# Optimization experiments

Measured on AMD Instinct MI355X. Metric: run time of the kernel, lower is better.

The kernel has to match this reference:

```python
import jax, jax.numpy as jnp
import numpy as np

LOG2 = 0.6931471805599453  # shifted_softplus(x) = softplus(x) - log(2)
NUM_MOL = 20_000  # static maxm for segment reduction


def ssp(x):
    return jax.nn.softplus(x) - LOG2


def setup_inputs() -> dict:
    key = jax.random.key(0)
    ks = jax.random.split(key, 5)
    N, D, H, E, M = 1_000_000, 128, 64, 4, NUM_MOL
    x = jax.random.normal(ks[0], (N, D), dtype=jnp.float32)
    zidx = jax.random.randint(ks[1], (N,), 0, E, dtype=jnp.int32)
    idx_m = jnp.sort(jax.random.randint(ks[2], (N,), 0, M, dtype=jnp.int32))
    # stacked per-element pyramidal MLP params: D -> D//2 -> 1
    W1 = jax.random.normal(ks[3], (E, D, H), dtype=jnp.float32) * (1.0 / np.sqrt(D))
    b1 = jnp.zeros((E, H), dtype=jnp.float32)
    W2 = jax.random.normal(ks[4], (E, H, 1), dtype=jnp.float32) * (1.0 / np.sqrt(H))
    b2 = jnp.zeros((E, 1), dtype=jnp.float32)
    return dict(x=x, zidx=zidx, idx_m=idx_m, W1=W1, b1=b1, W2=W2, b2=b2)


def reference(x, zidx, idx_m, W1, b1, W2, b2):
    # ElementwiseMLP: run each element's 2-layer MLP, select per atom by element.
    E = W1.shape[0]
    yi = jnp.zeros((x.shape[0], W2.shape[-1]), dtype=x.dtype)  # [N, n_out]
    for e in range(E):  # small fixed element set
        h = ssp(x @ W1[e] + b1[e])            # [N, H]
        ye = h @ W2[e] + b2[e]                # [N, n_out]
        yi = yi + jnp.where((zidx == e)[:, None], ye, jnp.zeros((), dtype=x.dtype))
    # aggregation_mode == 'sum': index_add per molecule
    y = jax.ops.segment_sum(yi, idx_m, num_segments=NUM_MOL)  # [M, n_out]
    return jnp.squeeze(y, -1)  # [M]
```

## Files before the change

kernel.cpp:

```cpp
#include <hip/hip_runtime.h>

typedef _Float16 half8 __attribute__((ext_vector_type(8)));
typedef float f32x4 __attribute__((ext_vector_type(4)));

#define LDSROW 136

__global__ __launch_bounds__(256, 2)
void elemental_atomwise_kernel(const float* __restrict__ x,
                               const int* __restrict__ zidx,
                               const int* __restrict__ idx_m,
                               const float* __restrict__ W1,
                               const float* __restrict__ b1,
                               const float* __restrict__ W2,
                               const float* __restrict__ b2,
                               float* __restrict__ y,
                               int N) {
  extern __shared__ _Float16 w1t[];

#pragma unroll
  for (int it = 0; it < 32; ++it) {
    int idx4 = threadIdx.x + it * 256;
    f32x4 v = ((const f32x4*)W1)[idx4];
    int lin = idx4 << 2;
    int e = lin >> 13;
    int d = (lin >> 6) & 127;
    int h = lin & 63;
    int n = e * 64 + h;
#pragma unroll
    for (int j = 0; j < 4; ++j)
      w1t[(n + j) * LDSROW + d] = (_Float16)v[j];
  }
  __syncthreads();

  const int lane = threadIdx.x & 63;
  const int wave = threadIdx.x >> 6;
  const int c = lane & 15;
  const int q = lane >> 4;
  const long tile = (long)blockIdx.x * 4 + wave;
  const long base = tile * 64;
  if (base >= N) return;

  int ameta = (base + lane < N) ? (int)(base + lane) : (N - 1);
  const int zvec = zidx[ameta];
  const int ivec = idx_m[ameta];

  half8 af[4][4];
#pragma unroll
  for (int mt = 0; mt < 4; ++mt) {
    long row = base + mt * 16 + c;
    if (row >= N) row = N - 1;
    const f32x4* rp = (const f32x4*)(x + row * 128);
#pragma unroll
    for (int kt = 0; kt < 4; ++kt) {
      f32x4 u0 = rp[kt * 8 + q * 2];
      f32x4 u1 = rp[kt * 8 + q * 2 + 1];
      half8 a;
      a[0] = (_Float16)u0[0]; a[1] = (_Float16)u0[1];
      a[2] = (_Float16)u0[2]; a[3] = (_Float16)u0[3];
      a[4] = (_Float16)u1[0]; a[5] = (_Float16)u1[1];
      a[6] = (_Float16)u1[2]; a[7] = (_Float16)u1[3];
      af[mt][kt] = a;
    }
  }

#pragma unroll
  for (int e = 0; e < 4; ++e) {
    f32x4 acc[4][4];
#pragma unroll
    for (int mt = 0; mt < 4; ++mt)
#pragma unroll
      for (int nt = 0; nt < 4; ++nt)
        acc[mt][nt] = (f32x4){0.f, 0.f, 0.f, 0.f};

#pragma unroll
    for (int kt = 0; kt < 4; ++kt) {
#pragma unroll
      for (int nt = 0; nt < 4; ++nt) {
        half8 bf = *(const half8*)&w1t[(e * 64 + nt * 16 + c) * LDSROW + kt * 32 + q * 8];
#pragma unroll
        for (int mt = 0; mt < 4; ++mt)
          acc[mt][nt] = __builtin_amdgcn_mfma_f32_16x16x32_f16(af[mt][kt], bf, acc[mt][nt], 0, 0, 0);
      }
    }

    float b1v[4], w2v[4];
#pragma unroll
    for (int nt = 0; nt < 4; ++nt) {
      b1v[nt] = b1[e * 64 + nt * 16 + c];
      w2v[nt] = W2[e * 64 + nt * 16 + c];
    }
    const float b2e = b2[e];
#pragma unroll
    for (int mt = 0; mt < 4; ++mt) {
#pragma unroll
      for (int i = 0; i < 4; ++i) {
        float s = 0.0f;
#pragma unroll
        for (int nt = 0; nt < 4; ++nt) {
          float t = acc[mt][nt][i] + b1v[nt];
          float hsp = __logf(1.0f + __expf(t)) - 0.69314718056f;
          s = fmaf(hsp, w2v[nt], s);
        }
        s += __shfl_xor(s, 1);
        s += __shfl_xor(s, 2);
        s += __shfl_xor(s, 4);
        s += __shfl_xor(s, 8);
        int mloc = mt * 16 + q * 4 + i;
        int zm = __shfl(zvec, mloc);
        int im = __shfl(ivec, mloc);
        if (c == 0 && zm == e && base + mloc < N)
          atomicAdd(&y[im], s + b2e);
      }
    }
  }
}

extern "C" void kernel_launch(void* const* d_in, const int* in_sizes, int n_in,
                              void* d_out, int out_size, void* d_ws, size_t ws_size,
                              hipStream_t stream) {
  const float* x = (const float*)d_in[0];
  const int* zidx = (const int*)d_in[1];
  const int* idx_m = (const int*)d_in[2];
  const float* W1 = (const float*)d_in[3];
  const float* b1 = (const float*)d_in[4];
  const float* W2 = (const float*)d_in[5];
  const float* b2 = (const float*)d_in[6];
  float* y = (float*)d_out;

  const int N = in_sizes[0] / 128;

  hipMemsetAsync(d_out, 0, (size_t)out_size * sizeof(float), stream);

  const int tiles = (N + 63) / 64;
  const int blocks = (tiles + 3) / 4;
  const size_t lds_bytes = 256 * LDSROW * sizeof(_Float16);

  elemental_atomwise_kernel<<<blocks, 256, lds_bytes, stream>>>(
      x, zidx, idx_m, W1, b1, W2, b2, y, N);
}
```

Measured before the change: 836.0 us.

## Assign one element per wave with register-resident weights and persistent grid

Changes the work split so each of the four waves in a block owns one element's W1 slice, held in registers as fp16 fragments, and all four waves process the same 64-atom tile. A persistent grid of 512 blocks strides over tiles, so the LDS staging of W1 and the per-block prologue are paid once per block rather than once per 64×4 atoms. The costs are that each x tile is now read by four waves (relying on L2/L1 reuse), every wave computes only its element, register pressure rises from 64 extra VGPRs of weight fragments, and the strided per-element W1 global loads are uncoalesced at startup.

```diff
diff --git a/kernel.cpp b/kernel.cpp
--- a/kernel.cpp
+++ b/kernel.cpp
@@ -2,8 +2,6 @@
 
 typedef _Float16 half8 __attribute__((ext_vector_type(8)));
 typedef float f32x4 __attribute__((ext_vector_type(4)));
-
-#define LDSROW 136
 
 __global__ __launch_bounds__(256, 2)
 void elemental_atomwise_kernel(const float* __restrict__ x,
@@ -14,57 +12,39 @@
                                const float* __restrict__ W2,
                                const float* __restrict__ b2,
                                float* __restrict__ y,
-                               int N) {
-  extern __shared__ _Float16 w1t[];
-
-#pragma unroll
-  for (int it = 0; it < 32; ++it) {
-    int idx4 = threadIdx.x + it * 256;
-    f32x4 v = ((const f32x4*)W1)[idx4];
-    int lin = idx4 << 2;
-    int e = lin >> 13;
-    int d = (lin >> 6) & 127;
-    int h = lin & 63;
-    int n = e * 64 + h;
-#pragma unroll
-    for (int j = 0; j < 4; ++j)
-      w1t[(n + j) * LDSROW + d] = (_Float16)v[j];
-  }
-  __syncthreads();
-
+                               int N, int ntiles) {
   const int lane = threadIdx.x & 63;
-  const int wave = threadIdx.x >> 6;
+  const int e = threadIdx.x >> 6;
   const int c = lane & 15;
   const int q = lane >> 4;
-  const long tile = (long)blockIdx.x * 4 + wave;
-  const long base = tile * 64;
-  if (base >= N) return;
 
-  int ameta = (base + lane < N) ? (int)(base + lane) : (N - 1);
-  const int zvec = zidx[ameta];
-  const int ivec = idx_m[ameta];
+  half8 bf[4][4];
+#pragma unroll
+  for (int kt = 0; kt < 4; ++kt)
+#pragma unroll
+    for (int nt = 0; nt < 4; ++nt) {
+      const float* wp = W1 + e * 8192 + (kt * 32 + q * 8) * 64 + nt * 16 + c;
+      half8 b;
+#pragma unroll
+      for (int j = 0; j < 8; ++j) b[j] = (_Float16)wp[j * 64];
+      bf[kt][nt] = b;
+    }
+  float b1v[4], w2v[4];
+#pragma unroll
+  for (int nt = 0; nt < 4; ++nt) {
+    b1v[nt] = b1[e * 64 + nt * 16 + c];
+    w2v[nt] = W2[e * 64 + nt * 16 + c];
+  }
+  const float b2e = b2[e];
 
-  half8 af[4][4];
-#pragma unroll
-  for (int mt = 0; mt < 4; ++mt) {
-    long row = base + mt * 16 + c;
-    if (row >= N) row = N - 1;
-    const f32x4* rp = (const f32x4*)(x + row * 128);
-#pragma unroll
-    for (int kt = 0; kt < 4; ++kt) {
-      f32x4 u0 = rp[kt * 8 + q * 2];
-      f32x4 u1 = rp[kt * 8 + q * 2 + 1];
-      half8 a;
-      a[0] = (_Float16)u0[0]; a[1] = (_Float16)u0[1];
-      a[2] = (_Float16)u0[2]; a[3] = (_Float16)u0[3];
-      a[4] = (_Float16)u1[0]; a[5] = (_Float16)u1[1];
-      a[6] = (_Float16)u1[2]; a[7] = (_Float16)u1[3];
-      af[mt][kt] = a;
-    }
-  }
+  for (int tile = blockIdx.x; tile < ntiles; tile += gridDim.x) {
+    const long base = (long)tile * 64;
 
-#pragma unroll
-  for (int e = 0; e < 4; ++e) {
+    long mi = base + lane;
+    if (mi >= N) mi = N - 1;
+    const int zm_l = zidx[mi];
+    const int im_l = idx_m[mi];
+
     f32x4 acc[4][4];
 #pragma unroll
     for (int mt = 0; mt < 4; ++mt)
@@ -74,22 +54,29 @@
 
 #pragma unroll
     for (int kt = 0; kt < 4; ++kt) {
+      half8 af[4];
 #pragma unroll
-      for (int nt = 0; nt < 4; ++nt) {
-        half8 bf = *(const half8*)&w1t[(e * 64 + nt * 16 + c) * LDSROW + kt * 32 + q * 8];
+      for (int mt = 0; mt < 4; ++mt) {
+        long row = base + mt * 16 + c;
+        if (row >= N) row = N - 1;
+        const f32x4* rp = (const f32x4*)(x + row * 128);
+        f32x4 u0 = rp[kt * 8 + q * 2];
+        f32x4 u1 = rp[kt * 8 + q * 2 + 1];
+        half8 a;
+        a[0] = (_Float16)u0[0]; a[1] = (_Float16)u0[1];
+        a[2] = (_Float16)u0[2]; a[3] = (_Float16)u0[3];
+        a[4] = (_Float16)u1[0]; a[5] = (_Float16)u1[1];
+        a[6] = (_Float16)u1[2]; a[7] = (_Float16)u1[3];
+        af[mt] = a;
+      }
+#pragma unroll
+      for (int nt = 0; nt < 4; ++nt)
 #pragma unroll
         for (int mt = 0; mt < 4; ++mt)
-          acc[mt][nt] = __builtin_amdgcn_mfma_f32_16x16x32_f16(af[mt][kt], bf, acc[mt][nt], 0, 0, 0);
-      }
+          acc[mt][nt] = __builtin_amdgcn_mfma_f32_16x16x32_f16(
+              af[mt], bf[kt][nt], acc[mt][nt], 0, 0, 0);
     }
 
-    float b1v[4], w2v[4];
-#pragma unroll
-    for (int nt = 0; nt < 4; ++nt) {
-      b1v[nt] = b1[e * 64 + nt * 16 + c];
-      w2v[nt] = W2[e * 64 + nt * 16 + c];
-    }
-    const float b2e = b2[e];
 #pragma unroll
     for (int mt = 0; mt < 4; ++mt) {
 #pragma unroll
@@ -98,16 +85,16 @@
 #pragma unroll
         for (int nt = 0; nt < 4; ++nt) {
           float t = acc[mt][nt][i] + b1v[nt];
-          float hsp = __logf(1.0f + __expf(t)) - 0.69314718056f;
-          s = fmaf(hsp, w2v[nt], s);
+          float sp = __logf(1.0f + __expf(t)) - 0.69314718056f;
+          s = fmaf(sp, w2v[nt], s);
         }
         s += __shfl_xor(s, 1);
         s += __shfl_xor(s, 2);
         s += __shfl_xor(s, 4);
         s += __shfl_xor(s, 8);
-        int mloc = mt * 16 + q * 4 + i;
-        int zm = __shfl(zvec, mloc);
-        int im = __shfl(ivec, mloc);
+        const int mloc = mt * 16 + q * 4 + i;
+        const int zm = __shfl(zm_l, mloc);
+        const int im = __shfl(im_l, mloc);
         if (c == 0 && zm == e && base + mloc < N)
           atomicAdd(&y[im], s + b2e);
       }
@@ -128,13 +115,13 @@
   float* y = (float*)d_out;
 
   const int N = in_sizes[0] / 128;
+  const int ntiles = (N + 63) / 64;
 
   hipMemsetAsync(d_out, 0, (size_t)out_size * sizeof(float), stream);
 
-  const int tiles = (N + 63) / 64;
-  const int blocks = (tiles + 3) / 4;
-  const size_t lds_bytes = 256 * LDSROW * sizeof(_Float16);
+  int blocks = 512;
+  if (blocks > ntiles) blocks = ntiles;
 
-  elemental_atomwise_kernel<<<blocks, 256, lds_bytes, stream>>>(
-      x, zidx, idx_m, W1, b1, W2, b2, y, N);
+  elemental_atomwise_kernel<<<blocks, 256, 0, stream>>>(
+      x, zidx, idx_m, W1, b1, W2, b2, y, N, ntiles);
 }
```

Result: slower. 972.8 us (+16.4%).
